# Performance work log

Hardware: AMD Instinct MI355X
Metric: run time of the kernel (lower is better)

Reference implementation:

```python
import jax, jax.numpy as jnp
import numpy as np

D_MODEL = 128
EXPAND = 8
D_INNER = EXPAND * D_MODEL            # 1024
HEADDIM = D_MODEL                     # headdim = int(in_channels*8/8)
NHEADS = D_INNER // HEADDIM           # 8
D_STATE = 128
D_CONV = 4
CONV_DIM = D_INNER + 2 * D_STATE      # 1280
D_IN_PROJ = 2 * D_INNER + 2 * D_STATE + NHEADS  # 2312
EPS = 1e-5
B_SZ, SEQ = 2, 2048


def setup_inputs() -> dict:
    key = jax.random.key(0)
    ks = jax.random.split(key, 16)
    n = jax.random.normal
    dt_init = jax.random.uniform(ks[4], (NHEADS,), minval=0.001, maxval=0.1)
    return dict(
        hidden_states=n(ks[0], (B_SZ, SEQ, D_MODEL), jnp.float32),
        w_in=n(ks[1], (D_IN_PROJ, D_MODEL), jnp.float32) / np.float32(np.sqrt(D_MODEL)),
        conv_w=n(ks[2], (CONV_DIM, D_CONV), jnp.float32) / np.float32(np.sqrt(D_CONV)),
        conv_b=n(ks[3], (CONV_DIM,), jnp.float32) * 0.01,
        dt_bias=jnp.log(jnp.expm1(dt_init)),  # inverse-softplus init (official)
        A_log=jnp.log(jax.random.uniform(ks[5], (NHEADS,), minval=1.0, maxval=16.0)),
        D_skip=jnp.ones((NHEADS,), jnp.float32),
        gnorm_w=jnp.ones((D_INNER,), jnp.float32),
        w_out=n(ks[6], (D_MODEL, D_INNER), jnp.float32) / np.float32(np.sqrt(D_INNER)),
        ln1_w=jnp.ones((D_MODEL,), jnp.float32),
        ln1_b=jnp.zeros((D_MODEL,), jnp.float32),
        ln2_w=jnp.ones((D_MODEL,), jnp.float32),
        ln2_b=jnp.zeros((D_MODEL,), jnp.float32),
        mlp_w=n(ks[7], (D_MODEL, D_MODEL), jnp.float32) / np.float32(np.sqrt(D_MODEL)),
        mlp_b=jnp.zeros((D_MODEL,), jnp.float32),
    )


def _layer_norm(x, w, b):
    m = x.mean(-1, keepdims=True)
    xc = x - m
    v = (xc * xc).mean(-1, keepdims=True)
    return xc * jax.lax.rsqrt(v + EPS) * w + b


def _mixer(u, w_in, conv_w, conv_b, dt_bias, A_log, D_skip, gnorm_w, w_out):
    b, l, _ = u.shape
    zxbcdt = u @ w_in.T                                    # (b,l,2312)
    z = zxbcdt[..., :D_INNER]                              # gate
    xBC = zxbcdt[..., D_INNER:D_INNER + CONV_DIM]
    dt = jax.nn.softplus(zxbcdt[..., -NHEADS:] + dt_bias)  # (b,l,h)
    # depthwise causal conv1d + SiLU
    xc = jnp.pad(xBC.swapaxes(1, 2), ((0, 0), (0, 0), (D_CONV - 1, 0)))
    xc = jax.lax.conv_general_dilated(xc, conv_w[:, None, :], (1,), 'VALID',
                                      feature_group_count=CONV_DIM)
    xBC = jax.nn.silu((xc + conv_b[None, :, None]).swapaxes(1, 2))
    x = xBC[..., :D_INNER].reshape(b, l, NHEADS, HEADDIM)  # (b,l,h,p)
    Bm = xBC[..., D_INNER:D_INNER + D_STATE]               # (b,l,n), ngroups=1
    Cm = xBC[..., D_INNER + D_STATE:]                      # (b,l,n)
    A = -jnp.exp(A_log)                                    # (h,)
    dA = jnp.exp(dt * A)                                   # (b,l,h)

    def step(S, inp):
        dA_t, dt_t, B_t, C_t, x_t = inp
        S = S * dA_t[:, :, None, None] + jnp.einsum('bh,bhp,bn->bhpn', dt_t, x_t, B_t)
        return S, jnp.einsum('bhpn,bn->bhp', S, C_t)

    S0 = jnp.zeros((b, NHEADS, HEADDIM, D_STATE), u.dtype)
    _, ys = jax.lax.scan(step, S0, (dA.swapaxes(0, 1), dt.swapaxes(0, 1),
                                    Bm.swapaxes(0, 1), Cm.swapaxes(0, 1),
                                    x.swapaxes(0, 1)))
    y = ys.swapaxes(0, 1) + D_skip[None, None, :, None] * x  # skip connection
    y = y.reshape(b, l, D_INNER) * jax.nn.silu(z)            # gated RMSNorm
    y = y * jax.lax.rsqrt((y * y).mean(-1, keepdims=True) + EPS) * gnorm_w
    return y @ w_out.T


def reference(hidden_states, w_in, conv_w, conv_b, dt_bias, A_log, D_skip,
              gnorm_w, w_out, ln1_w, ln1_b, ln2_w, ln2_b, mlp_w, mlp_b):
    residual = hidden_states
    h = _layer_norm(residual, ln1_w, ln1_b)
    h = _mixer(h, w_in, conv_w, conv_b, dt_bias, A_log, D_skip, gnorm_w, w_out)
    residual = h + residual
    h = _layer_norm(residual, ln2_w, ln2_b)
    return h @ mlp_w.T + mlp_b
```

## Files before the change

kernel.cpp:

```cpp
#include <hip/hip_runtime.h>
#include <hip/hip_bf16.h>

#define B_SZ 2
#define SEQ 2048
#define DMODEL 128
#define DINNER 1024
#define NHEADS 8
#define HEADDIM 128
#define DSTATE 128
#define CONVDIM 1280
#define NPROJ 2304
#define NTOK (B_SZ*SEQ)
#define CHUNK 64
#define NCHUNK (SEQ/CHUNK)
#define LDT 72

using bf16_t = __hip_bfloat16;
using short8 = __attribute__((ext_vector_type(8))) short;
using short4v= __attribute__((ext_vector_type(4))) short;
using f32x4  = __attribute__((ext_vector_type(4))) float;

__device__ __forceinline__ float silu_f(float x) { return x / (1.f + expf(-x)); }
__device__ __forceinline__ float bf2f(short s) {
    unsigned u = ((unsigned)(unsigned short)s) << 16;
    return __uint_as_float(u);
}
__device__ __forceinline__ short f2bf_s(float f) {
    bf16_t h = __float2bfloat16(f);
    return *(short*)&h;
}

__global__ __launch_bounds__(128) void head_fused(
        const float* __restrict__ hidden,
        const float* __restrict__ ln1_w, const float* __restrict__ ln1_b,
        const float* __restrict__ w_in,
        const float* __restrict__ dt_bias, const float* __restrict__ A_log,
        bf16_t* __restrict__ h_bf, float* __restrict__ dtb, float* __restrict__ ldAb,
        const float* __restrict__ wa, int na, const float* __restrict__ wb, int nb,
        const float* __restrict__ wc, int nc,
        bf16_t* __restrict__ oa, bf16_t* __restrict__ ob, bf16_t* __restrict__ oc) {
    int blk = blockIdx.x;
    if (blk >= NTOK) {
        int i = (blk - NTOK) * 128 + threadIdx.x;
        if (i < na) oa[i] = __float2bfloat16(wa[i]);
        else if (i < na + nb) ob[i - na] = __float2bfloat16(wb[i - na]);
        else if (i < na + nb + nc) oc[i - na - nb] = __float2bfloat16(wc[i - na - nb]);
        return;
    }
    int m = blk, t = threadIdx.x;
    __shared__ float red[128];
    __shared__ float sred[2][8];
    float v = hidden[(size_t)m*DMODEL + t];
    red[t] = v; __syncthreads();
    for (int s = 64; s > 0; s >>= 1) { if (t < s) red[t] += red[t+s]; __syncthreads(); }
    float mean = red[0] * (1.f/128.f);
    __syncthreads();
    float xc = v - mean;
    red[t] = xc * xc; __syncthreads();
    for (int s = 64; s > 0; s >>= 1) { if (t < s) red[t] += red[t+s]; __syncthreads(); }
    float var = red[0] * (1.f/128.f);
    float o = xc * rsqrtf(var + 1e-5f) * ln1_w[t] + ln1_b[t];
    h_bf[(size_t)m*DMODEL + t] = __float2bfloat16(o);
    int wave = t >> 6, lane = t & 63;
#pragma unroll
    for (int hd = 0; hd < NHEADS; hd++) {
        float p = o * w_in[(size_t)(NPROJ + hd)*DMODEL + t];
#pragma unroll
        for (int d = 1; d < 64; d <<= 1) p += __shfl_xor(p, d, 64);
        if (lane == 0) sred[wave][hd] = p;
    }
    __syncthreads();
    if (t < NHEADS) {
        float s = sred[0][t] + sred[1][t] + dt_bias[t];
        float dtv = (s > 20.f) ? s : log1pf(expf(s));
        float Av = -expf(A_log[t]);
        dtb[m*NHEADS + t] = dtv;
        ldAb[m*NHEADS + t] = dtv * Av;
    }
}

__global__ __launch_bounds__(256) void gemm_bf(const bf16_t* __restrict__ A,
                                               const bf16_t* __restrict__ W,
                                               bf16_t* __restrict__ C,
                                               int M, int N, int K) {
    int tid = threadIdx.x;
    int wave = tid >> 6, lane = tid & 63;
    int m0 = blockIdx.x * 64 + wave * 16;
    int n0 = blockIdx.y * 64;
    int lr = lane & 15, quad = lane >> 4;
    f32x4 acc[4];
#pragma unroll
    for (int j = 0; j < 4; j++) acc[j] = (f32x4){0.f, 0.f, 0.f, 0.f};
    for (int k0 = 0; k0 < K; k0 += 32) {
        short8 a = *(const short8*)(A + (size_t)(m0 + lr)*K + k0 + quad*8);
#pragma unroll
        for (int j = 0; j < 4; j++) {
            short8 b = *(const short8*)(W + (size_t)(n0 + j*16 + lr)*K + k0 + quad*8);
            acc[j] = __builtin_amdgcn_mfma_f32_16x16x32_bf16(a, b, acc[j], 0, 0, 0);
        }
    }
#pragma unroll
    for (int j = 0; j < 4; j++)
#pragma unroll
        for (int r = 0; r < 4; r++) {
            int row = m0 + quad*4 + r;
            int col = n0 + j*16 + lr;
            C[(size_t)row*N + col] = __float2bfloat16(acc[j][r]);
        }
}

__global__ __launch_bounds__(256) void conv_silu(const bf16_t* __restrict__ zxb,
                                                 const float* __restrict__ conv_w,
                                                 const float* __restrict__ conv_b,
                                                 bf16_t* __restrict__ xBCb) {
    int idx = blockIdx.x * 256 + threadIdx.x;
    if (idx >= NTOK * CONVDIM / 4) return;
    int c4 = (idx % (CONVDIM/4)) * 4;
    int m  = idx / (CONVDIM/4);
    int b = m >> 11, l = m & (SEQ - 1);
    float acc[4];
    f32x4 wv[4];
#pragma unroll
    for (int j = 0; j < 4; j++) {
        acc[j] = conv_b[c4 + j];
        wv[j] = *(const f32x4*)(conv_w + (c4 + j)*4);
    }
#pragma unroll
    for (int k = 0; k < 4; k++) {
        int ll = l - 3 + k;
        if (ll >= 0) {
            short4v v = *(const short4v*)(zxb + (size_t)(b*SEQ + ll)*NPROJ + DINNER + c4);
#pragma unroll
            for (int j = 0; j < 4; j++) acc[j] += bf2f(v[j]) * wv[j][k];
        }
    }
    short4v res;
#pragma unroll
    for (int j = 0; j < 4; j++) res[j] = f2bf_s(silu_f(acc[j]));
    *(short4v*)(xBCb + (size_t)m*CONVDIM + c4) = res;
}

__global__ __launch_bounds__(256) void scanA_mfma(const bf16_t* __restrict__ xBCb,
                                                  const float* __restrict__ dt,
                                                  const float* __restrict__ ldA,
                                                  bf16_t* __restrict__ Sloc,
                                                  float* __restrict__ Pbuf) {
    int bid = blockIdx.x;
    int c = bid & 31, hd = (bid >> 5) & 7, b = bid >> 8;
    int t = threadIdx.x, wave = t >> 6, lane = t & 63;
    int lr = lane & 15, quad = lane >> 4;
    __shared__ bf16_t XT[128*LDT];
    __shared__ bf16_t BT[128*LDT];
    __shared__ float ws[CHUNK];
    int m0tok = b*SEQ + c*CHUNK;
    if (t < 64) {
        float L = ldA[(m0tok + t)*NHEADS + hd];
#pragma unroll
        for (int d = 1; d < 64; d <<= 1) {
            float u = __shfl_up(L, d, 64);
            if (lane >= d) L += u;
        }
        float Ltot = __shfl(L, 63, 64);
        ws[t] = expf(Ltot - L) * dt[(m0tok + t)*NHEADS + hd];
        if (t == 63) Pbuf[bid] = expf(Ltot);
    }
    __syncthreads();
#pragma unroll 4
    for (int i = 0; i < 32; i++) {
        int idx = i*256 + t;
        int tt = idx >> 7, p = idx & 127;
        const bf16_t* row = xBCb + (size_t)(m0tok + tt)*CONVDIM;
        float xv = bf2f(*(const short*)&row[hd*HEADDIM + p]);
        XT[p*LDT + tt] = __float2bfloat16(xv * ws[tt]);
        BT[p*LDT + tt] = row[DINNER + p];
    }
    __syncthreads();
    int m0w = wave * 32;
    f32x4 acc[2][8];
#pragma unroll
    for (int mi = 0; mi < 2; mi++)
#pragma unroll
        for (int ni = 0; ni < 8; ni++) acc[mi][ni] = (f32x4){0.f,0.f,0.f,0.f};
#pragma unroll
    for (int k0 = 0; k0 < 64; k0 += 32) {
        short8 a[2];
#pragma unroll
        for (int mi = 0; mi < 2; mi++)
            a[mi] = *(const short8*)&XT[(m0w + mi*16 + lr)*LDT + k0 + quad*8];
#pragma unroll
        for (int ni = 0; ni < 8; ni++) {
            short8 bb = *(const short8*)&BT[(ni*16 + lr)*LDT + k0 + quad*8];
#pragma unroll
            for (int mi = 0; mi < 2; mi++)
                acc[mi][ni] = __builtin_amdgcn_mfma_f32_16x16x32_bf16(a[mi], bb, acc[mi][ni], 0, 0, 0);
        }
    }
    bf16_t* outp = Sloc + (size_t)bid * 16384;
#pragma unroll
    for (int mi = 0; mi < 2; mi++)
#pragma unroll
        for (int ni = 0; ni < 8; ni++)
#pragma unroll
            for (int r = 0; r < 4; r++) {
                int p = m0w + mi*16 + quad*4 + r;
                int n = ni*16 + lr;
                outp[p*128 + n] = __float2bfloat16(acc[mi][ni][r]);
            }
}

__global__ __launch_bounds__(256) void scanB(const bf16_t* __restrict__ Sloc,
                                             bf16_t* __restrict__ Sini,
                                             const float* __restrict__ Pbuf) {
    int bid = blockIdx.x;
    int bh = bid >> 5, slice = bid & 31;
    int t = threadIdx.x;
    int off = slice*512 + t*2;
    size_t base = (size_t)bh * NCHUNK * 16384;
    float run0 = 0.f, run1 = 0.f;
    for (int cc = 0; cc < NCHUNK; cc++) {
        unsigned raw = *(const unsigned*)(Sloc + base + (size_t)cc*16384 + off);
        float P = Pbuf[bh*NCHUNK + cc];
        unsigned o0 = (unsigned)(unsigned short)f2bf_s(run0);
        unsigned o1 = (unsigned)(unsigned short)f2bf_s(run1);
        *(unsigned*)(Sini + base + (size_t)cc*16384 + off) = o0 | (o1 << 16);
        run0 = run0*P + bf2f((short)(raw & 0xffff));
        run1 = run1*P + bf2f((short)(raw >> 16));
    }
}

__global__ __launch_bounds__(256) void scanC_mfma(const bf16_t* __restrict__ xBCb,
                                                  const float* __restrict__ dt,
                                                  const float* __restrict__ ldA,
                                                  const bf16_t* __restrict__ Sini,
                                                  const float* __restrict__ Dskip,
                                                  bf16_t* __restrict__ ybuf) {
    int bid = blockIdx.x;
    int c = bid & 31, hd = (bid >> 5) & 7, b = bid >> 8;
    int t = threadIdx.x, wave = t >> 6, lane = t & 63;
    int lr = lane & 15, quad = lane >> 4;
    __shared__ bf16_t XT[128*LDT];
    __shared__ bf16_t Mlds[64*LDT];
    __shared__ float Ls[CHUNK], dts[CHUNK];
    int m0tok = b*SEQ + c*CHUNK;
    if (t < 64) {
        float L = ldA[(m0tok + t)*NHEADS + hd];
#pragma unroll
        for (int d = 1; d < 64; d <<= 1) {
            float u = __shfl_up(L, d, 64);
            if (lane >= d) L += u;
        }
        Ls[t] = L;
        dts[t] = dt[(m0tok + t)*NHEADS + hd];
    }
#pragma unroll 4
    for (int i = 0; i < 32; i++) {
        int idx = i*256 + t;
        int tt = idx >> 7, p = idx & 127;
        XT[p*LDT + tt] = xBCb[(size_t)(m0tok + tt)*CONVDIM + hd*HEADDIM + p];
    }
    __syncthreads();
    const bf16_t* Crow = xBCb + (size_t)m0tok*CONVDIM + DINNER + DSTATE;
    const bf16_t* Brow = xBCb + (size_t)m0tok*CONVDIM + DINNER;
    f32x4 g[4];
#pragma unroll
    for (int si = 0; si < 4; si++) g[si] = (f32x4){0.f,0.f,0.f,0.f};
#pragma unroll
    for (int k0 = 0; k0 < 128; k0 += 32) {
        short8 a = *(const short8*)(Crow + (size_t)(wave*16 + lr)*CONVDIM + k0 + quad*8);
#pragma unroll
        for (int si = 0; si < 4; si++) {
            short8 bb = *(const short8*)(Brow + (size_t)(si*16 + lr)*CONVDIM + k0 + quad*8);
            g[si] = __builtin_amdgcn_mfma_f32_16x16x32_bf16(a, bb, g[si], 0, 0, 0);
        }
    }
#pragma unroll
    for (int si = 0; si < 4; si++)
#pragma unroll
        for (int r = 0; r < 4; r++) {
            int tt = wave*16 + quad*4 + r;
            int ss = si*16 + lr;
            float v = (ss <= tt) ? g[si][r] * expf(Ls[tt] - Ls[ss]) * dts[ss] : 0.f;
            Mlds[tt*LDT + ss] = __float2bfloat16(v);
        }
    __syncthreads();
    int p0 = wave * 32;
    f32x4 acc[4][2];
#pragma unroll
    for (int mi = 0; mi < 4; mi++)
#pragma unroll
        for (int ni = 0; ni < 2; ni++) acc[mi][ni] = (f32x4){0.f,0.f,0.f,0.f};
    const bf16_t* Sb = Sini + (size_t)bid * 16384;
#pragma unroll
    for (int k0 = 0; k0 < 128; k0 += 32) {
        short8 aC[4];
#pragma unroll
        for (int mi = 0; mi < 4; mi++)
            aC[mi] = *(const short8*)(Crow + (size_t)(mi*16 + lr)*CONVDIM + k0 + quad*8);
#pragma unroll
        for (int ni = 0; ni < 2; ni++) {
            short8 bb = *(const short8*)(Sb + (size_t)(p0 + ni*16 + lr)*128 + k0 + quad*8);
#pragma unroll
            for (int mi = 0; mi < 4; mi++)
                acc[mi][ni] = __builtin_amdgcn_mfma_f32_16x16x32_bf16(aC[mi], bb, acc[mi][ni], 0, 0, 0);
        }
    }
#pragma unroll
    for (int mi = 0; mi < 4; mi++) {
        float el[4];
#pragma unroll
        for (int r = 0; r < 4; r++) el[r] = expf(Ls[mi*16 + quad*4 + r]);
#pragma unroll
        for (int ni = 0; ni < 2; ni++)
#pragma unroll
            for (int r = 0; r < 4; r++) acc[mi][ni][r] *= el[r];
    }
#pragma unroll
    for (int k0 = 0; k0 < 64; k0 += 32) {
        short8 aM[4];
#pragma unroll
        for (int mi = 0; mi < 4; mi++)
            aM[mi] = *(const short8*)&Mlds[(mi*16 + lr)*LDT + k0 + quad*8];
#pragma unroll
        for (int ni = 0; ni < 2; ni++) {
            short8 bb = *(const short8*)&XT[(p0 + ni*16 + lr)*LDT + k0 + quad*8];
#pragma unroll
            for (int mi = 0; mi < 4; mi++)
                acc[mi][ni] = __builtin_amdgcn_mfma_f32_16x16x32_bf16(aM[mi], bb, acc[mi][ni], 0, 0, 0);
        }
    }
    float dsk = Dskip[hd];
#pragma unroll
    for (int mi = 0; mi < 4; mi++)
#pragma unroll
        for (int ni = 0; ni < 2; ni++)
#pragma unroll
            for (int r = 0; r < 4; r++) {
                int tt = mi*16 + quad*4 + r;
                int pp = p0 + ni*16 + lr;
                float xv = bf2f(*(const short*)&XT[pp*LDT + tt]);
                int m = m0tok + tt;
                ybuf[(size_t)m*DINNER + hd*HEADDIM + pp] = __float2bfloat16(acc[mi][ni][r] + dsk*xv);
            }
}

__global__ __launch_bounds__(256) void gate_out_mlp(const bf16_t* __restrict__ ybuf,
                                                    const bf16_t* __restrict__ zxb,
                                                    const float* __restrict__ gw,
                                                    const bf16_t* __restrict__ Wb,
                                                    const float* __restrict__ resid,
                                                    const float* __restrict__ w2,
                                                    const float* __restrict__ b2,
                                                    const bf16_t* __restrict__ Wm,
                                                    const float* __restrict__ mb,
                                                    float* __restrict__ out) {
    int blk = blockIdx.x, t = threadIdx.x;
    int tok0 = blk * 16;
    int tt = t >> 4, cg = t & 15;
    __shared__ bf16_t A1[16*1032];
    __shared__ float MIX[16*132];
    __shared__ bf16_t A2[16*136];
    {
        int ch0 = cg * 64;
        const bf16_t* yr = ybuf + (size_t)(tok0 + tt)*DINNER + ch0;
        const bf16_t* zr = zxb  + (size_t)(tok0 + tt)*NPROJ  + ch0;
        float vals[64];
        float ss = 0.f;
#pragma unroll
        for (int i = 0; i < 64; i += 4) {
            short4v y = *(const short4v*)(yr + i);
            short4v z = *(const short4v*)(zr + i);
#pragma unroll
            for (int r = 0; r < 4; r++) {
                float v = bf2f(y[r]) * silu_f(bf2f(z[r]));
                vals[i + r] = v; ss += v*v;
            }
        }
#pragma unroll
        for (int d = 1; d < 16; d <<= 1) ss += __shfl_xor(ss, d, 64);
        float rstd = rsqrtf(ss*(1.f/1024.f) + 1e-5f);
#pragma unroll
        for (int i = 0; i < 64; i += 4) {
            short4v pk;
#pragma unroll
            for (int r = 0; r < 4; r++) pk[r] = f2bf_s(vals[i+r]*rstd*gw[ch0+i+r]);
            *(short4v*)&A1[tt*1032 + ch0 + i] = pk;
        }
    }
    __syncthreads();
    int wave = t >> 6, lane = t & 63, lr = lane & 15, quad = lane >> 4;
    {
        f32x4 acc[2];
        acc[0] = (f32x4){0.f,0.f,0.f,0.f}; acc[1] = (f32x4){0.f,0.f,0.f,0.f};
        for (int k0 = 0; k0 < 1024; k0 += 32) {
            short8 a = *(const short8*)&A1[lr*1032 + k0 + quad*8];
#pragma unroll
            for (int j = 0; j < 2; j++) {
                int col = wave*32 + j*16 + lr;
                short8 bb = *(const short8*)(Wb + (size_t)col*DINNER + k0 + quad*8);
                acc[j] = __builtin_amdgcn_mfma_f32_16x16x32_bf16(a, bb, acc[j], 0, 0, 0);
            }
        }
#pragma unroll
        for (int j = 0; j < 2; j++)
#pragma unroll
            for (int r = 0; r < 4; r++)
                MIX[(quad*4 + r)*132 + wave*32 + j*16 + lr] = acc[j][r];
    }
    __syncthreads();
    {
        int ch0 = cg * 8;
        const float* rr = resid + (size_t)(tok0 + tt)*DMODEL + ch0;
        float v[8];
        f32x4 r0 = *(const f32x4*)rr, r1 = *(const f32x4*)(rr + 4);
#pragma unroll
        for (int r = 0; r < 4; r++) {
            v[r]   = MIX[tt*132 + ch0 + r]     + r0[r];
            v[4+r] = MIX[tt*132 + ch0 + 4 + r] + r1[r];
        }
        float s = 0.f, sq = 0.f;
#pragma unroll
        for (int i = 0; i < 8; i++) { s += v[i]; sq += v[i]*v[i]; }
#pragma unroll
        for (int d = 1; d < 16; d <<= 1) { s += __shfl_xor(s, d, 64); sq += __shfl_xor(sq, d, 64); }
        float mean = s * (1.f/128.f);
        float var  = sq * (1.f/128.f) - mean*mean;
        float rstd = rsqrtf(var + 1e-5f);
        short4v p0, p1;
#pragma unroll
        for (int r = 0; r < 4; r++) {
            p0[r] = f2bf_s((v[r]   - mean)*rstd*w2[ch0+r]   + b2[ch0+r]);
            p1[r] = f2bf_s((v[4+r] - mean)*rstd*w2[ch0+4+r] + b2[ch0+4+r]);
        }
        *(short4v*)&A2[tt*136 + ch0]     = p0;
        *(short4v*)&A2[tt*136 + ch0 + 4] = p1;
    }
    __syncthreads();
    {
        f32x4 acc[2];
        acc[0] = (f32x4){0.f,0.f,0.f,0.f}; acc[1] = (f32x4){0.f,0.f,0.f,0.f};
#pragma unroll
        for (int k0 = 0; k0 < 128; k0 += 32) {
            short8 a = *(const short8*)&A2[lr*136 + k0 + quad*8];
#pragma unroll
            for (int j = 0; j < 2; j++) {
                int col = wave*32 + j*16 + lr;
                short8 bb = *(const short8*)(Wm + (size_t)col*DMODEL + k0 + quad*8);
                acc[j] = __builtin_amdgcn_mfma_f32_16x16x32_bf16(a, bb, acc[j], 0, 0, 0);
            }
        }
#pragma unroll
        for (int j = 0; j < 2; j++)
#pragma unroll
            for (int r = 0; r < 4; r++) {
                int row = tok0 + quad*4 + r;
                int col = wave*32 + j*16 + lr;
                out[(size_t)row*DMODEL + col] = acc[j][r] + mb[col];
            }
    }
}

extern "C" void kernel_launch(void* const* d_in, const int* in_sizes, int n_in,
                              void* d_out, int out_size, void* d_ws, size_t ws_size,
                              hipStream_t stream) {
    const float* hidden  = (const float*)d_in[0];
    const float* w_in    = (const float*)d_in[1];
    const float* conv_w  = (const float*)d_in[2];
    const float* conv_b  = (const float*)d_in[3];
    const float* dt_bias = (const float*)d_in[4];
    const float* A_log   = (const float*)d_in[5];
    const float* D_skip  = (const float*)d_in[6];
    const float* gnorm_w = (const float*)d_in[7];
    const float* w_out   = (const float*)d_in[8];
    const float* ln1_w   = (const float*)d_in[9];
    const float* ln1_b   = (const float*)d_in[10];
    const float* ln2_w   = (const float*)d_in[11];
    const float* ln2_b   = (const float*)d_in[12];
    const float* mlp_w   = (const float*)d_in[13];
    const float* mlp_b   = (const float*)d_in[14];
    float* out = (float*)d_out;

    char* ws = (char*)d_ws;
    size_t off = 0;
    auto alloc = [&](size_t bytes) -> void* {
        void* p = ws + off;
        off = (off + bytes + 255) & ~(size_t)255;
        return p;
    };
    bf16_t* h_bf   = (bf16_t*)alloc((size_t)NTOK*DMODEL*2);
    bf16_t* w_in_bf= (bf16_t*)alloc((size_t)NPROJ*DMODEL*2);
    bf16_t* w_out_bf=(bf16_t*)alloc((size_t)DMODEL*DINNER*2);
    bf16_t* mlp_bf = (bf16_t*)alloc((size_t)DMODEL*DMODEL*2);
    bf16_t* zx_bf  = (bf16_t*)alloc((size_t)NTOK*NPROJ*2);
    bf16_t* xBCb   = (bf16_t*)alloc((size_t)NTOK*CONVDIM*2);
    float*  dtb    = (float*) alloc((size_t)NTOK*NHEADS*4);
    float*  ldAb   = (float*) alloc((size_t)NTOK*NHEADS*4);
    bf16_t* Sloc   = (bf16_t*)alloc((size_t)B_SZ*NHEADS*NCHUNK*16384*2);
    bf16_t* Sini   = (bf16_t*)alloc((size_t)B_SZ*NHEADS*NCHUNK*16384*2);
    float*  Pbuf   = (float*) alloc((size_t)B_SZ*NHEADS*NCHUNK*4);
    bf16_t* ybuf   = (bf16_t*)alloc((size_t)NTOK*DINNER*2);
    (void)ws_size; (void)in_sizes; (void)n_in; (void)out_size;

    {
        int na = NPROJ*DMODEL, nb = DMODEL*DINNER, nc = DMODEL*DMODEL;
        int castBlocks = (na + nb + nc + 127) / 128;
        head_fused<<<NTOK + castBlocks, 128, 0, stream>>>(
            hidden, ln1_w, ln1_b, w_in, dt_bias, A_log, h_bf, dtb, ldAb,
            w_in, na, w_out, nb, mlp_w, nc, w_in_bf, w_out_bf, mlp_bf);
    }
    gemm_bf<<<dim3(NTOK/64, NPROJ/64), 256, 0, stream>>>(h_bf, w_in_bf, zx_bf,
                                                         NTOK, NPROJ, DMODEL);
    conv_silu<<<((size_t)NTOK*CONVDIM/4 + 255)/256, 256, 0, stream>>>(zx_bf, conv_w, conv_b, xBCb);
    scanA_mfma<<<B_SZ*NHEADS*NCHUNK, 256, 0, stream>>>(xBCb, dtb, ldAb, Sloc, Pbuf);
    scanB<<<B_SZ*NHEADS*NCHUNK, 256, 0, stream>>>(Sloc, Sini, Pbuf);
    scanC_mfma<<<B_SZ*NHEADS*NCHUNK, 256, 0, stream>>>(xBCb, dtb, ldAb, Sini, D_skip, ybuf);
    gate_out_mlp<<<NTOK/16, 256, 0, stream>>>(ybuf, zx_bf, gnorm_w, w_out_bf,
                                              hidden, ln2_w, ln2_b, mlp_bf, mlp_b, out);
}
```

Before: 184.7 us.

## Double SSD chunk length to 128 and restructure scan kernels for larger chunks

```diff
diff --git a/kernel.cpp b/kernel.cpp
--- a/kernel.cpp
+++ b/kernel.cpp
@@ -11,7 +11,7 @@
 #define CONVDIM 1280
 #define NPROJ 2304
 #define NTOK (B_SZ*SEQ)
-#define CHUNK 64
+#define CHUNK 128
 #define NCHUNK (SEQ/CHUNK)
 #define LDT 72
 
@@ -146,53 +146,65 @@
                                                   bf16_t* __restrict__ Sloc,
                                                   float* __restrict__ Pbuf) {
     int bid = blockIdx.x;
-    int c = bid & 31, hd = (bid >> 5) & 7, b = bid >> 8;
+    int c = bid & 15, hd = (bid >> 4) & 7, b = bid >> 7;
     int t = threadIdx.x, wave = t >> 6, lane = t & 63;
     int lr = lane & 15, quad = lane >> 4;
     __shared__ bf16_t XT[128*LDT];
     __shared__ bf16_t BT[128*LDT];
     __shared__ float ws[CHUNK];
+    __shared__ float wtot[2];
     int m0tok = b*SEQ + c*CHUNK;
-    if (t < 64) {
-        float L = ldA[(m0tok + t)*NHEADS + hd];
+    float dtv = 0.f, Lv = 0.f;
+    if (t < 128) {
+        dtv = dt[(m0tok + t)*NHEADS + hd];
+        Lv  = ldA[(m0tok + t)*NHEADS + hd];
 #pragma unroll
         for (int d = 1; d < 64; d <<= 1) {
-            float u = __shfl_up(L, d, 64);
-            if (lane >= d) L += u;
-        }
-        float Ltot = __shfl(L, 63, 64);
-        ws[t] = expf(Ltot - L) * dt[(m0tok + t)*NHEADS + hd];
-        if (t == 63) Pbuf[bid] = expf(Ltot);
-    }
-    __syncthreads();
+            float u = __shfl_up(Lv, d, 64);
+            if (lane >= d) Lv += u;
+        }
+        if (lane == 63) wtot[t >> 6] = Lv;
+    }
+    __syncthreads();
+    float Ltot = wtot[0] + wtot[1];
+    if (t < 128) {
+        float L = Lv + ((t >= 64) ? wtot[0] : 0.f);
+        ws[t] = expf(Ltot - L) * dtv;
+    }
+    if (t == 0) Pbuf[bid] = expf(Ltot);
+    __syncthreads();
+    f32x4 acc[2][8];
+#pragma unroll
+    for (int mi = 0; mi < 2; mi++)
+#pragma unroll
+        for (int ni = 0; ni < 8; ni++) acc[mi][ni] = (f32x4){0.f,0.f,0.f,0.f};
+    int m0w = wave * 32;
+#pragma unroll
+    for (int kp = 0; kp < 2; kp++) {
+        if (kp) __syncthreads();
 #pragma unroll 4
-    for (int i = 0; i < 32; i++) {
-        int idx = i*256 + t;
-        int tt = idx >> 7, p = idx & 127;
-        const bf16_t* row = xBCb + (size_t)(m0tok + tt)*CONVDIM;
-        float xv = bf2f(*(const short*)&row[hd*HEADDIM + p]);
-        XT[p*LDT + tt] = __float2bfloat16(xv * ws[tt]);
-        BT[p*LDT + tt] = row[DINNER + p];
-    }
-    __syncthreads();
-    int m0w = wave * 32;
-    f32x4 acc[2][8];
-#pragma unroll
-    for (int mi = 0; mi < 2; mi++)
-#pragma unroll
-        for (int ni = 0; ni < 8; ni++) acc[mi][ni] = (f32x4){0.f,0.f,0.f,0.f};
-#pragma unroll
-    for (int k0 = 0; k0 < 64; k0 += 32) {
-        short8 a[2];
-#pragma unroll
-        for (int mi = 0; mi < 2; mi++)
-            a[mi] = *(const short8*)&XT[(m0w + mi*16 + lr)*LDT + k0 + quad*8];
-#pragma unroll
-        for (int ni = 0; ni < 8; ni++) {
-            short8 bb = *(const short8*)&BT[(ni*16 + lr)*LDT + k0 + quad*8];
+        for (int i = 0; i < 32; i++) {
+            int idx = i*256 + t;
+            int tt = idx >> 7, p = idx & 127;
+            const bf16_t* row = xBCb + (size_t)(m0tok + kp*64 + tt)*CONVDIM;
+            float xv = bf2f(*(const short*)&row[hd*HEADDIM + p]);
+            XT[p*LDT + tt] = __float2bfloat16(xv * ws[kp*64 + tt]);
+            BT[p*LDT + tt] = row[DINNER + p];
+        }
+        __syncthreads();
+#pragma unroll
+        for (int k0 = 0; k0 < 64; k0 += 32) {
+            short8 a[2];
 #pragma unroll
             for (int mi = 0; mi < 2; mi++)
-                acc[mi][ni] = __builtin_amdgcn_mfma_f32_16x16x32_bf16(a[mi], bb, acc[mi][ni], 0, 0, 0);
+                a[mi] = *(const short8*)&XT[(m0w + mi*16 + lr)*LDT + k0 + quad*8];
+#pragma unroll
+            for (int ni = 0; ni < 8; ni++) {
+                short8 bb = *(const short8*)&BT[(ni*16 + lr)*LDT + k0 + quad*8];
+#pragma unroll
+                for (int mi = 0; mi < 2; mi++)
+                    acc[mi][ni] = __builtin_amdgcn_mfma_f32_16x16x32_bf16(a[mi], bb, acc[mi][ni], 0, 0, 0);
+            }
         }
     }
     bf16_t* outp = Sloc + (size_t)bid * 16384;
@@ -212,19 +224,21 @@
                                              bf16_t* __restrict__ Sini,
                                              const float* __restrict__ Pbuf) {
     int bid = blockIdx.x;
-    int bh = bid >> 5, slice = bid & 31;
+    int bh = bid >> 4, slice = bid & 15;
     int t = threadIdx.x;
-    int off = slice*512 + t*2;
+    int off = slice*1024 + t*4;
     size_t base = (size_t)bh * NCHUNK * 16384;
-    float run0 = 0.f, run1 = 0.f;
+    float run[4] = {0.f, 0.f, 0.f, 0.f};
     for (int cc = 0; cc < NCHUNK; cc++) {
-        unsigned raw = *(const unsigned*)(Sloc + base + (size_t)cc*16384 + off);
+        short4v raw = *(const short4v*)(Sloc + base + (size_t)cc*16384 + off);
         float P = Pbuf[bh*NCHUNK + cc];
-        unsigned o0 = (unsigned)(unsigned short)f2bf_s(run0);
-        unsigned o1 = (unsigned)(unsigned short)f2bf_s(run1);
-        *(unsigned*)(Sini + base + (size_t)cc*16384 + off) = o0 | (o1 << 16);
-        run0 = run0*P + bf2f((short)(raw & 0xffff));
-        run1 = run1*P + bf2f((short)(raw >> 16));
+        short4v outv;
+#pragma unroll
+        for (int i = 0; i < 4; i++) {
+            outv[i] = f2bf_s(run[i]);
+            run[i] = run[i]*P + bf2f(raw[i]);
+        }
+        *(short4v*)(Sini + base + (size_t)cc*16384 + off) = outv;
     }
 }
 
@@ -235,77 +249,58 @@
                                                   const float* __restrict__ Dskip,
                                                   bf16_t* __restrict__ ybuf) {
     int bid = blockIdx.x;
-    int c = bid & 31, hd = (bid >> 5) & 7, b = bid >> 8;
+    int c = bid & 15, hd = (bid >> 4) & 7, b = bid >> 7;
     int t = threadIdx.x, wave = t >> 6, lane = t & 63;
     int lr = lane & 15, quad = lane >> 4;
     __shared__ bf16_t XT[128*LDT];
-    __shared__ bf16_t Mlds[64*LDT];
+    __shared__ bf16_t Mlds[128*LDT];
     __shared__ float Ls[CHUNK], dts[CHUNK];
+    __shared__ float wtot[2];
     int m0tok = b*SEQ + c*CHUNK;
-    if (t < 64) {
-        float L = ldA[(m0tok + t)*NHEADS + hd];
-#pragma unroll
-        for (int d = 1; d < 64; d <<= 1) {
-            float u = __shfl_up(L, d, 64);
-            if (lane >= d) L += u;
-        }
-        Ls[t] = L;
-        dts[t] = dt[(m0tok + t)*NHEADS + hd];
-    }
-#pragma unroll 4
-    for (int i = 0; i < 32; i++) {
-        int idx = i*256 + t;
-        int tt = idx >> 7, p = idx & 127;
-        XT[p*LDT + tt] = xBCb[(size_t)(m0tok + tt)*CONVDIM + hd*HEADDIM + p];
-    }
-    __syncthreads();
+    {
+        float dtv = 0.f, Lv = 0.f;
+        if (t < 128) {
+            dtv = dt[(m0tok + t)*NHEADS + hd];
+            Lv  = ldA[(m0tok + t)*NHEADS + hd];
+#pragma unroll
+            for (int d = 1; d < 64; d <<= 1) {
+                float u = __shfl_up(Lv, d, 64);
+                if (lane >= d) Lv += u;
+            }
+            if (lane == 63) wtot[t >> 6] = Lv;
+        }
+        __syncthreads();
+        if (t < 128) {
+            Ls[t] = Lv + ((t >= 64) ? wtot[0] : 0.f);
+            dts[t] = dtv;
+        }
+        __syncthreads();
+    }
     const bf16_t* Crow = xBCb + (size_t)m0tok*CONVDIM + DINNER + DSTATE;
     const bf16_t* Brow = xBCb + (size_t)m0tok*CONVDIM + DINNER;
-    f32x4 g[4];
-#pragma unroll
-    for (int si = 0; si < 4; si++) g[si] = (f32x4){0.f,0.f,0.f,0.f};
-#pragma unroll
-    for (int k0 = 0; k0 < 128; k0 += 32) {
-        short8 a = *(const short8*)(Crow + (size_t)(wave*16 + lr)*CONVDIM + k0 + quad*8);
-#pragma unroll
-        for (int si = 0; si < 4; si++) {
-            short8 bb = *(const short8*)(Brow + (size_t)(si*16 + lr)*CONVDIM + k0 + quad*8);
-            g[si] = __builtin_amdgcn_mfma_f32_16x16x32_bf16(a, bb, g[si], 0, 0, 0);
-        }
-    }
-#pragma unroll
-    for (int si = 0; si < 4; si++)
-#pragma unroll
-        for (int r = 0; r < 4; r++) {
-            int tt = wave*16 + quad*4 + r;
-            int ss = si*16 + lr;
-            float v = (ss <= tt) ? g[si][r] * expf(Ls[tt] - Ls[ss]) * dts[ss] : 0.f;
-            Mlds[tt*LDT + ss] = __float2bfloat16(v);
-        }
-    __syncthreads();
     int p0 = wave * 32;
-    f32x4 acc[4][2];
-#pragma unroll
-    for (int mi = 0; mi < 4; mi++)
+    f32x4 acc[8][2];
+#pragma unroll
+    for (int mi = 0; mi < 8; mi++)
 #pragma unroll
         for (int ni = 0; ni < 2; ni++) acc[mi][ni] = (f32x4){0.f,0.f,0.f,0.f};
     const bf16_t* Sb = Sini + (size_t)bid * 16384;
 #pragma unroll
     for (int k0 = 0; k0 < 128; k0 += 32) {
-        short8 aC[4];
-#pragma unroll
-        for (int mi = 0; mi < 4; mi++)
+        short8 aC[8];
+#pragma unroll
+        for (int mi = 0; mi < 8; mi++)
             aC[mi] = *(const short8*)(Crow + (size_t)(mi*16 + lr)*CONVDIM + k0 + quad*8);
 #pragma unroll
         for (int ni = 0; ni < 2; ni++) {
             short8 bb = *(const short8*)(Sb + (size_t)(p0 + ni*16 + lr)*128 + k0 + quad*8);
 #pragma unroll
-            for (int mi = 0; mi < 4; mi++)
+            for (int mi = 0; mi < 8; mi++)
                 acc[mi][ni] = __builtin_amdgcn_mfma_f32_16x16x32_bf16(aC[mi], bb, acc[mi][ni], 0, 0, 0);
         }
     }
 #pragma unroll
-    for (int mi = 0; mi < 4; mi++) {
+    for (int mi = 0; mi < 8; mi++) {
         float el[4];
 #pragma unroll
         for (int r = 0; r < 4; r++) el[r] = expf(Ls[mi*16 + quad*4 + r]);
@@ -314,32 +309,78 @@
 #pragma unroll
             for (int r = 0; r < 4; r++) acc[mi][ni][r] *= el[r];
     }
-#pragma unroll
-    for (int k0 = 0; k0 < 64; k0 += 32) {
-        short8 aM[4];
-#pragma unroll
-        for (int mi = 0; mi < 4; mi++)
-            aM[mi] = *(const short8*)&Mlds[(mi*16 + lr)*LDT + k0 + quad*8];
-#pragma unroll
-        for (int ni = 0; ni < 2; ni++) {
-            short8 bb = *(const short8*)&XT[(p0 + ni*16 + lr)*LDT + k0 + quad*8];
-#pragma unroll
-            for (int mi = 0; mi < 4; mi++)
-                acc[mi][ni] = __builtin_amdgcn_mfma_f32_16x16x32_bf16(aM[mi], bb, acc[mi][ni], 0, 0, 0);
-        }
-    }
     float dsk = Dskip[hd];
 #pragma unroll
-    for (int mi = 0; mi < 4; mi++)
+    for (int h = 0; h < 2; h++) {
+        __syncthreads();
+#pragma unroll 4
+        for (int i = 0; i < 32; i++) {
+            int idx = i*256 + t;
+            int tt = idx >> 7, p = idx & 127;
+            XT[p*LDT + tt] = xBCb[(size_t)(m0tok + h*64 + tt)*CONVDIM + hd*HEADDIM + p];
+        }
+        __syncthreads();
+#pragma unroll
+        for (int p2 = 0; p2 < 2; p2++) {
+            int trow0 = p2*64 + wave*16;
+            f32x4 g[4];
+#pragma unroll
+            for (int si = 0; si < 4; si++) g[si] = (f32x4){0.f,0.f,0.f,0.f};
+#pragma unroll
+            for (int k0 = 0; k0 < 128; k0 += 32) {
+                short8 a = *(const short8*)(Crow + (size_t)(trow0 + lr)*CONVDIM + k0 + quad*8);
+#pragma unroll
+                for (int si = 0; si < 4; si++) {
+                    short8 bb = *(const short8*)(Brow + (size_t)(h*64 + si*16 + lr)*CONVDIM + k0 + quad*8);
+                    g[si] = __builtin_amdgcn_mfma_f32_16x16x32_bf16(a, bb, g[si], 0, 0, 0);
+                }
+            }
+#pragma unroll
+            for (int si = 0; si < 4; si++)
+#pragma unroll
+                for (int r = 0; r < 4; r++) {
+                    int tt = trow0 + quad*4 + r;
+                    int ssg = h*64 + si*16 + lr;
+                    float v = (ssg <= tt) ? g[si][r] * expf(Ls[tt] - Ls[ssg]) * dts[ssg] : 0.f;
+                    Mlds[tt*LDT + si*16 + lr] = __float2bfloat16(v);
+                }
+        }
+        __syncthreads();
+#pragma unroll
+        for (int k0 = 0; k0 < 64; k0 += 32) {
+            short8 aM[8];
+#pragma unroll
+            for (int mi = 0; mi < 8; mi++)
+                aM[mi] = *(const short8*)&Mlds[(mi*16 + lr)*LDT + k0 + quad*8];
+#pragma unroll
+            for (int ni = 0; ni < 2; ni++) {
+                short8 bb = *(const short8*)&XT[(p0 + ni*16 + lr)*LDT + k0 + quad*8];
+#pragma unroll
+                for (int mi = 0; mi < 8; mi++)
+                    acc[mi][ni] = __builtin_amdgcn_mfma_f32_16x16x32_bf16(aM[mi], bb, acc[mi][ni], 0, 0, 0);
+            }
+        }
+#pragma unroll
+        for (int mi = h*4; mi < h*4 + 4; mi++)
+#pragma unroll
+            for (int ni = 0; ni < 2; ni++)
+#pragma unroll
+                for (int r = 0; r < 4; r++) {
+                    int tloc = mi*16 + quad*4 + r - h*64;
+                    int pp = p0 + ni*16 + lr;
+                    acc[mi][ni][r] += dsk * bf2f(*(const short*)&XT[pp*LDT + tloc]);
+                }
+    }
+#pragma unroll
+    for (int mi = 0; mi < 8; mi++)
 #pragma unroll
         for (int ni = 0; ni < 2; ni++)
 #pragma unroll
             for (int r = 0; r < 4; r++) {
                 int tt = mi*16 + quad*4 + r;
                 int pp = p0 + ni*16 + lr;
-                float xv = bf2f(*(const short*)&XT[pp*LDT + tt]);
                 int m = m0tok + tt;
-                ybuf[(size_t)m*DINNER + hd*HEADDIM + pp] = __float2bfloat16(acc[mi][ni][r] + dsk*xv);
+                ybuf[(size_t)m*DINNER + hd*HEADDIM + pp] = __float2bfloat16(acc[mi][ni][r]);
             }
 }
 
@@ -425,14 +466,14 @@
         float mean = s * (1.f/128.f);
         float var  = sq * (1.f/128.f) - mean*mean;
         float rstd = rsqrtf(var + 1e-5f);
-        short4v p0, p1;
+        short4v p0v, p1v;
 #pragma unroll
         for (int r = 0; r < 4; r++) {
-            p0[r] = f2bf_s((v[r]   - mean)*rstd*w2[ch0+r]   + b2[ch0+r]);
-            p1[r] = f2bf_s((v[4+r] - mean)*rstd*w2[ch0+4+r] + b2[ch0+4+r]);
-        }
-        *(short4v*)&A2[tt*136 + ch0]     = p0;
-        *(short4v*)&A2[tt*136 + ch0 + 4] = p1;
+            p0v[r] = f2bf_s((v[r]   - mean)*rstd*w2[ch0+r]   + b2[ch0+r]);
+            p1v[r] = f2bf_s((v[4+r] - mean)*rstd*w2[ch0+4+r] + b2[ch0+4+r]);
+        }
+        *(short4v*)&A2[tt*136 + ch0]     = p0v;
+        *(short4v*)&A2[tt*136 + ch0 + 4] = p1v;
     }
     __syncthreads();
     {
@@ -511,7 +552,7 @@
                                                          NTOK, NPROJ, DMODEL);
     conv_silu<<<((size_t)NTOK*CONVDIM/4 + 255)/256, 256, 0, stream>>>(zx_bf, conv_w, conv_b, xBCb);
     scanA_mfma<<<B_SZ*NHEADS*NCHUNK, 256, 0, stream>>>(xBCb, dtb, ldAb, Sloc, Pbuf);
-    scanB<<<B_SZ*NHEADS*NCHUNK, 256, 0, stream>>>(Sloc, Sini, Pbuf);
+    scanB<<<B_SZ*NHEADS*16, 256, 0, stream>>>(Sloc, Sini, Pbuf);
     scanC_mfma<<<B_SZ*NHEADS*NCHUNK, 256, 0, stream>>>(xBCb, dtb, ldAb, Sini, D_skip, ybuf);
     gate_out_mlp<<<NTOK/16, 256, 0, stream>>>(ybuf, zx_bf, gnorm_w, w_out_bf,
                                               hidden, ln2_w, ln2_b, mlp_bf, mlp_b, out);
```

Result: no change. 186.9 us (+1.2%).
